# Performance work log

Measured on AMD Instinct MI355X. Metric: run time of the kernel, lower is better.

The kernel has to match this reference:

```python
import jax, jax.numpy as jnp
import numpy as np

B, C, F, D = 128, 16, 128, 512


def setup_inputs() -> dict:
    key = jax.random.key(0)
    k1, k2 = jax.random.split(key)
    return {
        "c_feats": jax.random.normal(k1, (B, C, D), dtype=jnp.float32),
        "f_feats": jax.random.normal(k2, (B, F, D), dtype=jnp.float32),
    }


def _dtw_path_masks(S):
    """S: [P, c, f] per-pair similarity. Returns [P, c, f] 0/1 max-path masks.

    DP: D[i,j] = max(D[i-1,j], D[i,j-1], D[i-1,j-1]) + S[i-1,j-1], D[0,0]=0,
    borders -inf. Tie-break priority (up, left, diag) matches Python max().
    Row recurrence is vectorized: D[i,j] = Csum[j] + cummax_k<=j(A[k]-Csum[k-1])
    where A[k]=max(D[i-1,k], D[i-1,k-1]) (wavefront-free row-parallel form).
    """
    P_, c, f = S.shape
    NEG = -jnp.inf

    init = jnp.concatenate([jnp.zeros((P_, 1), S.dtype),
                            jnp.full((P_, f), NEG, S.dtype)], axis=1)  # D[0, 0..f]

    def row_step(prev, dt_row):
        # prev: [P, f+1] = D[i-1, 0..f]; dt_row: [P, f] = S[i-1, :]
        A = jnp.maximum(prev[:, 1:], prev[:, :-1])                  # max(D[i-1,j], D[i-1,j-1])
        Ccum = jnp.cumsum(dt_row, axis=1)
        Cm1 = jnp.concatenate([jnp.zeros((P_, 1), dt_row.dtype), Ccum[:, :-1]], axis=1)
        row = Ccum + jax.lax.cummax(A - Cm1, axis=1)                # D[i, 1..f]
        new_prev = jnp.concatenate([jnp.full((P_, 1), NEG, dt_row.dtype), row], axis=1)
        return new_prev, new_prev

    _, rows = jax.lax.scan(row_step, init, jnp.moveaxis(S, 1, 0))   # [c, P, f+1]
    Dm = jnp.moveaxis(jnp.concatenate([init[None], rows], axis=0), 1, 0)  # [P, c+1, f+1]

    # Predecessor choice per cell; argmax picks first max -> priority up,left,diag
    up = Dm[:, :-1, 1:]
    left = Dm[:, 1:, :-1]
    diag = Dm[:, :-1, :-1]
    mv = jnp.argmax(jnp.stack([up, left, diag], axis=-1), axis=-1).astype(jnp.int32)
    mv = jnp.pad(mv, ((0, 0), (1, 0), (1, 0)))                      # [P, c+1, f+1]

    pidx = jnp.arange(P_)

    def bt_step(carry, _):
        mask, i, j = carry
        active = (i > 0) | (j > 0)
        mask = mask.at[pidx, i - 1, j - 1].add(jnp.where(active, 1.0, 0.0).astype(mask.dtype))
        m = mv[pidx, i, j]
        di = jnp.where(m == 1, 0, 1)   # left keeps i
        dj = jnp.where(m == 0, 0, 1)   # up keeps j
        i = jnp.where(active, i - di, i)
        j = jnp.where(active, j - dj, j)
        return (mask, i, j), None

    mask0 = jnp.zeros((P_, c, f), jnp.float32)
    i0 = jnp.full((P_,), c, jnp.int32)
    j0 = jnp.full((P_,), f, jnp.int32)
    (mask, _, _), _ = jax.lax.scan(bt_step, (mask0, i0, j0), None, length=c + f)
    return mask


def reference(c_feats, f_feats):
    b, c, d = c_feats.shape
    f = f_feats.shape[1]
    xn = c_feats / jnp.linalg.norm(c_feats, axis=-1, keepdims=True)
    yn = f_feats / jnp.linalg.norm(f_feats, axis=-1, keepdims=True)
    # Source quirk: y row j is normalized only once outer index i reaches it
    # (y[i-1] bug), so S[i,j] uses normalized y[j] iff j <= i, raw y[j] otherwise.
    Sn = jnp.einsum('mcd,nfd->mncf', xn, yn)
    Sr = jnp.einsum('mcd,nfd->mncf', xn, f_feats)
    tri = jnp.arange(f)[None, :] <= jnp.arange(c)[:, None]          # [c, f]: j <= i
    S = jnp.where(tri, Sn, Sr).reshape(b * b, c, f)
    return _dtw_path_masks(S).reshape(b, b, c, f)
```

## Files before the change

kernel.cpp:

```cpp
#include <hip/hip_runtime.h>
#include <stdint.h>

#define M_TOT 2048
#define N_TOT 16384
#define K_TOT 512

typedef _Float16 f16x8 __attribute__((ext_vector_type(8)));
typedef float f32x4 __attribute__((ext_vector_type(4)));
typedef float f32x16 __attribute__((ext_vector_type(16)));

#define AS1 __attribute__((address_space(1)))
#define AS3 __attribute__((address_space(3)))

__device__ __forceinline__ void ld_lds16(const void* g, void* l) {
    __builtin_amdgcn_global_load_lds((const AS1 void*)g, (AS3 void*)l, 16, 0, 0);
}

__device__ __forceinline__ void split4(float x0, float x1, float x2, float x3,
                                       uint2* hs, uint2* ls) {
    union U { _Float16 h[4]; uint2 u; } H, L;
    _Float16 h0 = (_Float16)x0; H.h[0] = h0; L.h[0] = (_Float16)(x0 - (float)h0);
    _Float16 h1 = (_Float16)x1; H.h[1] = h1; L.h[1] = (_Float16)(x1 - (float)h1);
    _Float16 h2 = (_Float16)x2; H.h[2] = h2; L.h[2] = (_Float16)(x2 - (float)h2);
    _Float16 h3 = (_Float16)x3; H.h[3] = h3; L.h[3] = (_Float16)(x3 - (float)h3);
    *hs = H.u; *ls = L.u;
}

__global__ __launch_bounds__(256) void norm_split_kernel(
    const float* __restrict__ c_feats, const float* __restrict__ f_feats,
    _Float16* __restrict__ Ah, _Float16* __restrict__ Al,
    _Float16* __restrict__ Bh, _Float16* __restrict__ Bl,
    float* __restrict__ normf)
{
    int wave = blockIdx.x * 4 + (threadIdx.x >> 6);
    int lane = threadIdx.x & 63;
    if (wave < 2048) {
        const float* row = c_feats + (size_t)wave * K_TOT;
        float4 v0 = ((const float4*)row)[lane];
        float4 v1 = ((const float4*)row)[lane + 64];
        double ss = (double)v0.x * v0.x + (double)v0.y * v0.y +
                    (double)v0.z * v0.z + (double)v0.w * v0.w +
                    (double)v1.x * v1.x + (double)v1.y * v1.y +
                    (double)v1.z * v1.z + (double)v1.w * v1.w;
        #pragma unroll
        for (int off = 32; off; off >>= 1) ss += __shfl_down(ss, off);
        double tot = __shfl(ss, 0);
        float nrm = sqrtf((float)tot);
        float a0 = v0.x / nrm, a1 = v0.y / nrm, a2 = v0.z / nrm, a3 = v0.w / nrm;
        float b0 = v1.x / nrm, b1 = v1.y / nrm, b2 = v1.z / nrm, b3 = v1.w / nrm;
        uint2 h, l;
        split4(a0, a1, a2, a3, &h, &l);
        ((uint2*)(Ah + (size_t)wave * K_TOT))[lane] = h;
        ((uint2*)(Al + (size_t)wave * K_TOT))[lane] = l;
        split4(b0, b1, b2, b3, &h, &l);
        ((uint2*)(Ah + (size_t)wave * K_TOT))[lane + 64] = h;
        ((uint2*)(Al + (size_t)wave * K_TOT))[lane + 64] = l;
    } else if (wave < 18432) {
        int fr = wave - 2048;
        const float* row = f_feats + (size_t)fr * K_TOT;
        float4 v0 = ((const float4*)row)[lane];
        float4 v1 = ((const float4*)row)[lane + 64];
        double ss = (double)v0.x * v0.x + (double)v0.y * v0.y +
                    (double)v0.z * v0.z + (double)v0.w * v0.w +
                    (double)v1.x * v1.x + (double)v1.y * v1.y +
                    (double)v1.z * v1.z + (double)v1.w * v1.w;
        #pragma unroll
        for (int off = 32; off; off >>= 1) ss += __shfl_down(ss, off);
        if (lane == 0) normf[fr] = sqrtf((float)ss);
        uint2 h, l;
        split4(v0.x, v0.y, v0.z, v0.w, &h, &l);
        ((uint2*)(Bh + (size_t)fr * K_TOT))[lane] = h;
        ((uint2*)(Bl + (size_t)fr * K_TOT))[lane] = l;
        split4(v1.x, v1.y, v1.z, v1.w, &h, &l);
        ((uint2*)(Bh + (size_t)fr * K_TOT))[lane + 64] = h;
        ((uint2*)(Bl + (size_t)fr * K_TOT))[lane + 64] = l;
    }
}

__global__ __launch_bounds__(256, 4) void mfma_gemm_kernel(
    const _Float16* __restrict__ Ah, const _Float16* __restrict__ Al,
    const _Float16* __restrict__ Bh, const _Float16* __restrict__ Bl,
    const float* __restrict__ normf,
    float* __restrict__ out)
{
    __shared__ _Float16 sAh[128 * 32];
    __shared__ _Float16 sAl[128 * 32];
    __shared__ _Float16 sBh[128 * 32];
    __shared__ _Float16 sBl[128 * 32];

    const int t = threadIdx.x;
    const int w = t >> 6, lane = t & 63;
    const int ntile = ((blockIdx.x & 7) << 4) | (blockIdx.x >> 3);
    const int gm0 = blockIdx.y * 128, gn0 = ntile * 128;
    const int wm = (w & 1) * 64, wn = (w >> 1) * 64;
    const int m32 = lane & 31;
    const int kql0 = lane >> 5;

    f32x16 acc[2][2] = {};
    const int l0 = w * 128 + lane;

    for (int k0 = 0; k0 < K_TOT; k0 += 32) {
        #pragma unroll
        for (int c = 0; c < 2; ++c) {
            int l = l0 + c * 64;
            int lrow = l >> 2, kq = l & 3;
            int kqs = kq ^ ((lrow >> 1) & 3);
            size_t goffA = (size_t)(gm0 + lrow) * K_TOT + k0 + kqs * 8;
            size_t goffB = (size_t)(gn0 + lrow) * K_TOT + k0 + kqs * 8;
            ld_lds16(Ah + goffA, sAh + (size_t)l * 8);
            ld_lds16(Al + goffA, sAl + (size_t)l * 8);
            ld_lds16(Bh + goffB, sBh + (size_t)l * 8);
            ld_lds16(Bl + goffB, sBl + (size_t)l * 8);
        }
        __syncthreads();

        #pragma unroll
        for (int kh = 0; kh < 2; ++kh) {
            f16x8 fah[2], fal[2], fbh[2], fbl[2];
            #pragma unroll
            for (int x = 0; x < 2; ++x) {
                int arr = wm + x * 32 + m32;
                int brr = wn + x * 32 + m32;
                int kqa = (kh * 2 + kql0) ^ ((arr >> 1) & 3);
                int kqb = (kh * 2 + kql0) ^ ((brr >> 1) & 3);
                int ar = arr * 32 + kqa * 8;
                int br = brr * 32 + kqb * 8;
                fah[x] = *(const f16x8*)(sAh + ar);
                fal[x] = *(const f16x8*)(sAl + ar);
                fbh[x] = *(const f16x8*)(sBh + br);
                fbl[x] = *(const f16x8*)(sBl + br);
            }
            #pragma unroll
            for (int mi = 0; mi < 2; ++mi)
                #pragma unroll
                for (int ni = 0; ni < 2; ++ni) {
                    acc[mi][ni] = __builtin_amdgcn_mfma_f32_32x32x16_f16(fah[mi], fbl[ni], acc[mi][ni], 0, 0, 0);
                    acc[mi][ni] = __builtin_amdgcn_mfma_f32_32x32x16_f16(fal[mi], fbh[ni], acc[mi][ni], 0, 0, 0);
                    acc[mi][ni] = __builtin_amdgcn_mfma_f32_32x32x16_f16(fah[mi], fbh[ni], acc[mi][ni], 0, 0, 0);
                }
        }
        __syncthreads();
    }

    const int nn = ntile;
    const int rq = 4 * (lane >> 5);
    #pragma unroll
    for (int ni = 0; ni < 2; ++ni) {
        int col = wn + ni * 32 + m32;
        bool cn = (col < 16);
        float nf = cn ? normf[gn0 + col] : 1.f;
        #pragma unroll
        for (int mi = 0; mi < 2; ++mi) {
            #pragma unroll
            for (int reg = 0; reg < 16; ++reg) {
                int r = wm + mi * 32 + (reg & 3) + 8 * (reg >> 2) + rq;
                int gm = gm0 + r;
                int mm = gm >> 4, ii = gm & 15;
                float v = acc[mi][ni][reg];
                if (cn && col <= ii) v /= nf;
                out[(((size_t)mm * 128 + nn) * 16 + ii) * 128 + col] = v;
            }
        }
    }
}

#define DQS 552
#define DBUFS 2208

__global__ __launch_bounds__(256) void dtw_kernel(float* __restrict__ buf)
{
    __shared__ float swin[4][2 * DBUFS];
    __shared__ uint32_t mvw[4][4][132];
    __shared__ int bounds[4][4][16];

    const int lane = threadIdx.x & 63;
    const int w = threadIdx.x >> 6;
    const int q = lane >> 4, r = lane & 15;
    const int pbase = (1023 - blockIdx.x) * 16 + w * 4;
    const float4* gbase = (const float4*)(buf + (size_t)pbase * 2048);
    float* sw = swin[w];
    uint32_t* mvq = &mvw[w][q][0];

    int gidx[8], lidx[8];
    #pragma unroll
    for (int i = 0; i < 8; ++i) {
        int f4 = i * 64 + lane;
        gidx[i] = (f4 >> 7) * 512 + ((f4 >> 3) & 15) * 32 + (f4 & 7);
        lidx[i] = (f4 >> 7) * DQS + ((f4 >> 3) & 15) * 34 + (f4 & 7) * 4;
    }

    float4 ga[8], gb[8];
    #pragma unroll
    for (int i = 0; i < 8; ++i) ga[i] = gbase[gidx[i]];
    #pragma unroll
    for (int i = 0; i < 8; ++i) gb[i] = gbase[gidx[i] + 8];
    #pragma unroll
    for (int i = 0; i < 8; ++i) {
        *(float2*)(sw + lidx[i])     = make_float2(ga[i].x, ga[i].y);
        *(float2*)(sw + lidx[i] + 2) = make_float2(ga[i].z, ga[i].w);
    }
    #pragma unroll
    for (int i = 0; i < 8; ++i) {
        *(float2*)(sw + DBUFS + lidx[i])     = make_float2(gb[i].x, gb[i].y);
        *(float2*)(sw + DBUFS + lidx[i] + 2) = make_float2(gb[i].z, gb[i].w);
    }
    #pragma unroll
    for (int i = 0; i < 8; ++i) ga[i] = gbase[gidx[i] + 16];
    __syncthreads();

    const double NEG = -1e300;
    double Dp = NEG, rawprev = NEG;
    uint32_t mvbuf = 0;
    int j = -r;
    const int sb = q * DQS + r * 34;

#define DTW_STEP(BOUNDARY)                                                      \
    {                                                                           \
        double upr = __shfl_up(Dp, 1);                                          \
        double dg = rawprev;                                                    \
        rawprev = upr;                                                          \
        double up = (r == 0) ? NEG : upr;                                       \
        double lf = Dp;                                                         \
        if (BOUNDARY) {                                                         \
            if (j == 0) { lf = NEG; dg = (r == 0) ? 0.0 : NEG; }                \
            else if (r == 0) dg = NEG;                                          \
        } else {                                                                \
            if (r == 0) dg = NEG;                                               \
        }                                                                       \
        float sv = sw[((j & 32) ? DBUFS : 0) + sb + (j & 31)];                  \
        int m = (up >= lf && up >= dg) ? 0 : ((lf >= dg) ? 1 : 2);              \
        double Dc = fmax(up, fmax(lf, dg)) + (double)sv;                        \
        if ((unsigned)j < 128u) {                                               \
            mvbuf |= (uint32_t)m << (2 * (j & 15));                             \
            if ((j & 15) == 15) { mvq[r * 8 + (j >> 4)] = mvbuf; mvbuf = 0; }   \
        }                                                                       \
        Dp = Dc;                                                                \
        ++j;                                                                    \
    }

    for (int t = 0; t < 16; ++t) DTW_STEP(true)
    for (int t = 16; t < 48; ++t) DTW_STEP(false)

    #pragma unroll
    for (int i = 0; i < 8; ++i) {
        *(float2*)(sw + lidx[i])     = make_float2(ga[i].x, ga[i].y);
        *(float2*)(sw + lidx[i] + 2) = make_float2(ga[i].z, ga[i].w);
    }
    #pragma unroll
    for (int i = 0; i < 8; ++i) gb[i] = gbase[gidx[i] + 24];
    __syncthreads();

    for (int t = 48; t < 80; ++t) DTW_STEP(false)

    #pragma unroll
    for (int i = 0; i < 8; ++i) {
        *(float2*)(sw + DBUFS + lidx[i])     = make_float2(gb[i].x, gb[i].y);
        *(float2*)(sw + DBUFS + lidx[i] + 2) = make_float2(gb[i].z, gb[i].w);
    }
    __syncthreads();

    for (int t = 80; t < 143; ++t) DTW_STEP(false)
#undef DTW_STEP

    __syncthreads();

    if (r == 0) {
        int i = 16, jj = 128, hic = 127;
        int cidx = -1;
        uint32_t word = 0;
        for (int it = 0; it < 160; ++it) {
            if (i <= 0) break;
            int idx = (i - 1) * 8 + ((jj - 1) >> 4);
            if (idx != cidx) { word = mvq[idx]; cidx = idx; }
            int m = (int)((word >> (2 * ((jj - 1) & 15))) & 3u);
            if (m == 1) { --jj; continue; }
            bounds[w][q][i - 1] = (jj - 1) | (hic << 8);
            if (m == 2) --jj;
            --i;
            hic = jj - 1;
        }
    }
    __syncthreads();

    #pragma unroll 4
    for (int it = 0; it < 32; ++it) {
        int flat = it * 64 + lane;
        int q2 = flat >> 9;
        int rem = flat & 511;
        int ii = rem >> 5;
        int c4 = rem & 31;
        int b = bounds[w][q2][ii];
        int lo = b & 0xff, hi = (b >> 8) & 0xff;
        int j0 = c4 * 4;
        float4 v;
        v.x = (j0 + 0 >= lo && j0 + 0 <= hi) ? 1.f : 0.f;
        v.y = (j0 + 1 >= lo && j0 + 1 <= hi) ? 1.f : 0.f;
        v.z = (j0 + 2 >= lo && j0 + 2 <= hi) ? 1.f : 0.f;
        v.w = (j0 + 3 >= lo && j0 + 3 <= hi) ? 1.f : 0.f;
        float* tb = buf + (size_t)(pbase + q2) * 2048;
        *(float4*)(tb + ii * 128 + j0) = v;
    }
}

extern "C" void kernel_launch(void* const* d_in, const int* in_sizes, int n_in,
                              void* d_out, int out_size, void* d_ws, size_t ws_size,
                              hipStream_t stream)
{
    const float* c_feats = (const float*)d_in[0];
    const float* f_feats = (const float*)d_in[1];
    float* out = (float*)d_out;

    _Float16* Ah = (_Float16*)d_ws;
    _Float16* Al = Ah + (size_t)M_TOT * K_TOT;
    _Float16* Bh = Al + (size_t)M_TOT * K_TOT;
    _Float16* Bl = Bh + (size_t)N_TOT * K_TOT;
    float* normf = (float*)(Bl + (size_t)N_TOT * K_TOT);

    norm_split_kernel<<<4608, 256, 0, stream>>>(c_feats, f_feats, Ah, Al, Bh, Bl, normf);
    dim3 g(N_TOT / 128, M_TOT / 128);
    mfma_gemm_kernel<<<g, 256, 0, stream>>>(Ah, Al, Bh, Bl, normf, out);
    dtw_kernel<<<1024, 256, 0, stream>>>(out);
}
```

Before: 354.2 us.

## Stream DTW similarity rows through 16-column double-buffered LDS windows without block syncs

The DTW kernel's per-wave LDS staging window shrinks from 32 to 16 columns, so staging now runs over eight smaller double-buffered windows. Each refill is interleaved every 16 wavefront steps, and the block-wide __syncthreads between stages are removed, since each wave owns its own buffer. This roughly halves LDS use and the staging registers, which should raise occupancy and remove barrier stalls. The cost is more frequent, smaller global loads interleaved with the recurrence, and correctness now relies on the lane skew never reading a buffer that has just been overwritten.

```diff
diff --git a/kernel.cpp b/kernel.cpp
--- a/kernel.cpp
+++ b/kernel.cpp
@@ -164,12 +164,12 @@
     }
 }
 
-#define DQS 552
-#define DBUFS 2208
+#define WQS 296
+#define WBUF 1184
 
 __global__ __launch_bounds__(256) void dtw_kernel(float* __restrict__ buf)
 {
-    __shared__ float swin[4][2 * DBUFS];
+    __shared__ float swin[4][2 * WBUF];
     __shared__ uint32_t mvw[4][4][132];
     __shared__ int bounds[4][4][16];
 
@@ -181,38 +181,40 @@
     float* sw = swin[w];
     uint32_t* mvq = &mvw[w][q][0];
 
-    int gidx[8], lidx[8];
+    int gidx[4], lidx[4];
     #pragma unroll
-    for (int i = 0; i < 8; ++i) {
-        int f4 = i * 64 + lane;
-        gidx[i] = (f4 >> 7) * 512 + ((f4 >> 3) & 15) * 32 + (f4 & 7);
-        lidx[i] = (f4 >> 7) * DQS + ((f4 >> 3) & 15) * 34 + (f4 & 7) * 4;
-    }
-
-    float4 ga[8], gb[8];
-    #pragma unroll
-    for (int i = 0; i < 8; ++i) ga[i] = gbase[gidx[i]];
-    #pragma unroll
-    for (int i = 0; i < 8; ++i) gb[i] = gbase[gidx[i] + 8];
-    #pragma unroll
-    for (int i = 0; i < 8; ++i) {
-        *(float2*)(sw + lidx[i])     = make_float2(ga[i].x, ga[i].y);
-        *(float2*)(sw + lidx[i] + 2) = make_float2(ga[i].z, ga[i].w);
-    }
-    #pragma unroll
-    for (int i = 0; i < 8; ++i) {
-        *(float2*)(sw + DBUFS + lidx[i])     = make_float2(gb[i].x, gb[i].y);
-        *(float2*)(sw + DBUFS + lidx[i] + 2) = make_float2(gb[i].z, gb[i].w);
-    }
-    #pragma unroll
-    for (int i = 0; i < 8; ++i) ga[i] = gbase[gidx[i] + 16];
-    __syncthreads();
+    for (int i = 0; i < 4; ++i) {
+        gidx[i] = i * 512 + ((lane >> 2) & 15) * 32 + (lane & 3);
+        lidx[i] = i * WQS + ((lane >> 2) & 15) * 18 + (lane & 3) * 4;
+    }
+
+#define WSTORE(regs, boff)                                                      \
+    {                                                                           \
+        _Pragma("unroll")                                                       \
+        for (int i = 0; i < 4; ++i) {                                           \
+            *(float2*)(sw + (boff) + lidx[i])     = make_float2(regs[i].x, regs[i].y); \
+            *(float2*)(sw + (boff) + lidx[i] + 2) = make_float2(regs[i].z, regs[i].w); \
+        }                                                                       \
+    }
+#define WLOAD(regs, win)                                                        \
+    {                                                                           \
+        _Pragma("unroll")                                                       \
+        for (int i = 0; i < 4; ++i) regs[i] = gbase[gidx[i] + (win) * 4];       \
+    }
+
+    float4 ga[4], gb[4];
+    WLOAD(ga, 0)
+    WLOAD(gb, 1)
+    WSTORE(ga, 0)
+    WSTORE(gb, WBUF)
+    WLOAD(ga, 2)
+    WLOAD(gb, 3)
 
     const double NEG = -1e300;
     double Dp = NEG, rawprev = NEG;
     uint32_t mvbuf = 0;
     int j = -r;
-    const int sb = q * DQS + r * 34;
+    const int sb = q * WQS + r * 18;
 
 #define DTW_STEP(BOUNDARY)                                                      \
     {                                                                           \
@@ -227,7 +229,7 @@
         } else {                                                                \
             if (r == 0) dg = NEG;                                               \
         }                                                                       \
-        float sv = sw[((j & 32) ? DBUFS : 0) + sb + (j & 31)];                  \
+        float sv = sw[(((j >> 4) & 1) ? WBUF : 0) + sb + (j & 15)];             \
         int m = (up >= lf && up >= dg) ? 0 : ((lf >= dg) ? 1 : 2);              \
         double Dc = fmax(up, fmax(lf, dg)) + (double)sv;                        \
         if ((unsigned)j < 128u) {                                               \
@@ -239,28 +241,22 @@
     }
 
     for (int t = 0; t < 16; ++t) DTW_STEP(true)
-    for (int t = 16; t < 48; ++t) DTW_STEP(false)
-
-    #pragma unroll
-    for (int i = 0; i < 8; ++i) {
-        *(float2*)(sw + lidx[i])     = make_float2(ga[i].x, ga[i].y);
-        *(float2*)(sw + lidx[i] + 2) = make_float2(ga[i].z, ga[i].w);
-    }
-    #pragma unroll
-    for (int i = 0; i < 8; ++i) gb[i] = gbase[gidx[i] + 24];
-    __syncthreads();
-
-    for (int t = 48; t < 80; ++t) DTW_STEP(false)
-
-    #pragma unroll
-    for (int i = 0; i < 8; ++i) {
-        *(float2*)(sw + DBUFS + lidx[i])     = make_float2(gb[i].x, gb[i].y);
-        *(float2*)(sw + DBUFS + lidx[i] + 2) = make_float2(gb[i].z, gb[i].w);
-    }
-    __syncthreads();
-
-    for (int t = 80; t < 143; ++t) DTW_STEP(false)
+    for (int t = 16; t < 32; ++t) DTW_STEP(false)
+    WSTORE(ga, 0)        WLOAD(ga, 4)
+    for (int t = 32; t < 48; ++t) DTW_STEP(false)
+    WSTORE(gb, WBUF)     WLOAD(gb, 5)
+    for (int t = 48; t < 64; ++t) DTW_STEP(false)
+    WSTORE(ga, 0)        WLOAD(ga, 6)
+    for (int t = 64; t < 80; ++t) DTW_STEP(false)
+    WSTORE(gb, WBUF)     WLOAD(gb, 7)
+    for (int t = 80; t < 96; ++t) DTW_STEP(false)
+    WSTORE(ga, 0)
+    for (int t = 96; t < 112; ++t) DTW_STEP(false)
+    WSTORE(gb, WBUF)
+    for (int t = 112; t < 143; ++t) DTW_STEP(false)
 #undef DTW_STEP
+#undef WSTORE
+#undef WLOAD
 
     __syncthreads();
 
```

After: 345.7 us. 1.02x faster.
